# Performance work log

Hardware: AMD Instinct MI355X
Metric: run time of the kernel (lower is better)

## Reference

```python
import jax, jax.numpy as jnp
import numpy as np

B, L, R, F = 16, 64, 256, 64
LIG_NIN, REC_NIN, EIN, EEMB = 32, 40, 16, 16
DEG = 8
E_LIG, E_REC = B * L * DEG, B * R * DEG
NL = 3
PNAMES = ["emb_nW", "emb_nb", "emb_eW", "emb_eb", "hidW", "hidb", "ln0_g", "ln0_b",
          "efW", "efb", "convb", "outW", "outb", "lng", "lnb"]
INT_NAMES = ("lig_src", "lig_dst", "rec_src", "rec_dst")


def _lrelu(v):
    return jax.nn.leaky_relu(v, 0.01)


def _ln(x, g, b):
    m = x.mean(-1, keepdims=True)
    v = ((x - m) ** 2).mean(-1, keepdims=True)
    return (x - m) / jnp.sqrt(v + 1e-5) * g + b


def _side(node_x, edge_x, src, dst, n_nodes, p):
    # GraphEmbedding: linear node/edge embedding
    eh = edge_x @ p["emb_eW"] + p["emb_eb"]                      # [E, EEMB]
    h = _lrelu(node_x @ p["emb_nW"] + p["emb_nb"]) @ p["hidW"] + p["hidb"]
    h = _ln(h, p["ln0_g"], p["ln0_b"])                           # [N, F]
    deg = jax.ops.segment_sum(jnp.ones(src.shape[0], jnp.float32), dst, num_segments=n_nodes)
    deg = jnp.maximum(deg, 1.0)[:, None]
    prev = []
    for i in range(NL):
        hh = _lrelu(h)
        # NNConv: per-edge F x F weight conditioned on edge features
        We = (eh @ p["efW"][i] + p["efb"][i]).reshape(-1, F, F)  # [E, F, F]
        msg = jnp.einsum('ei,eio->eo', hh[src], We)              # [E, F]
        agg = jax.ops.segment_sum(msg, dst, num_segments=n_nodes) / deg + p["convb"][i]
        h = _ln(_lrelu(agg) @ p["outW"][i] + p["outb"][i], p["lng"][i], p["lnb"][i])
        if i >= 2:  # residual to layer i-2
            h = h + prev[i - 2]
        prev.append(h)
    return h


def _forward(fl, lig_src, lig_dst, rec_src, rec_dst):
    lig_p = {n: fl["lig_" + n] for n in PNAMES}
    rec_p = {n: fl["rec_" + n] for n in PNAMES}
    lig_h = _side(fl["lig_x"], fl["lig_e"], lig_src, lig_dst, B * L, lig_p)
    rec_h = _side(fl["rec_x"], fl["rec_e"], rec_src, rec_dst, B * R, rec_p)
    # per-graph einsum('lf,rf->lr') scoring, batched since graphs are equal-sized
    op = jnp.einsum('blf,brf->blr', lig_h.reshape(B, L, F), rec_h.reshape(B, R, F))
    out = op.mean((1, 2))
    return out, op


def setup_inputs() -> dict:
    key = jax.random.key(0)
    it = iter(jax.random.split(key, 80))
    def nrm(shape, s=0.1):
        return jax.random.normal(next(it), shape, jnp.float32) * s
    inp = {}
    inp["lig_x"] = nrm((B * L, LIG_NIN), 1.0)
    inp["rec_x"] = nrm((B * R, REC_NIN), 1.0)
    inp["lig_e"] = nrm((E_LIG, EIN), 1.0)
    inp["rec_e"] = nrm((E_REC, EIN), 1.0)
    def edges(npg, epg, k1, k2):
        offs = (jnp.arange(B) * npg)[:, None]
        s = (jax.random.randint(k1, (B, epg), 0, npg) + offs).reshape(-1).astype(jnp.int32)
        d = (jax.random.randint(k2, (B, epg), 0, npg) + offs).reshape(-1).astype(jnp.int32)
        return s, d
    inp["lig_src"], inp["lig_dst"] = edges(L, L * DEG, next(it), next(it))
    inp["rec_src"], inp["rec_dst"] = edges(R, R * DEG, next(it), next(it))
    for pre, nin in (("lig", LIG_NIN), ("rec", REC_NIN)):
        inp[pre + "_emb_nW"] = nrm((nin, F)); inp[pre + "_emb_nb"] = nrm((F,))
        inp[pre + "_emb_eW"] = nrm((EIN, EEMB)); inp[pre + "_emb_eb"] = nrm((EEMB,))
        inp[pre + "_hidW"] = nrm((F, F)); inp[pre + "_hidb"] = nrm((F,))
        inp[pre + "_ln0_g"] = jnp.ones((F,)); inp[pre + "_ln0_b"] = jnp.zeros((F,))
        inp[pre + "_efW"] = nrm((NL, EEMB, F * F), 0.05); inp[pre + "_efb"] = nrm((NL, F * F), 0.05)
        inp[pre + "_convb"] = nrm((NL, F))
        inp[pre + "_outW"] = nrm((NL, F, F)); inp[pre + "_outb"] = nrm((NL, F))
        inp[pre + "_lng"] = jnp.ones((NL, F)); inp[pre + "_lnb"] = jnp.zeros((NL, F))
    return inp


def reference(lig_x, rec_x, lig_e, rec_e, lig_src, lig_dst, rec_src, rec_dst,
              lig_emb_nW, lig_emb_nb, lig_emb_eW, lig_emb_eb, lig_hidW, lig_hidb,
              lig_ln0_g, lig_ln0_b, lig_efW, lig_efb, lig_convb, lig_outW, lig_outb,
              lig_lng, lig_lnb,
              rec_emb_nW, rec_emb_nb, rec_emb_eW, rec_emb_eb, rec_hidW, rec_hidb,
              rec_ln0_g, rec_ln0_b, rec_efW, rec_efb, rec_convb, rec_outW, rec_outb,
              rec_lng, rec_lnb):
    all_args = dict(locals())
    fl = {k: v for k, v in all_args.items() if k not in INT_NAMES}
    return _forward(fl, lig_src, lig_dst, rec_src, rec_dst)
```

## Files before the change

kernel.cpp:

```cpp
#include <hip/hip_runtime.h>
#include <hip/hip_bf16.h>

#define NLIG 1024
#define NREC 4096
#define NTOT 5120
#define ELIG 8192
#define ETOT 40960
#define TPAD 1092

typedef __bf16 bf16x8 __attribute__((ext_vector_type(8)));
typedef float f32x4 __attribute__((ext_vector_type(4)));

struct Params {
  const float *lig_x, *rec_x, *lig_e, *rec_e;
  const int *lig_src, *lig_dst, *rec_src, *rec_dst;
  const float *nW[2], *nb[2], *eW[2], *eb[2], *hW[2], *hb[2], *g0[2], *b0[2];
  const float *efW[2], *efb[2], *convb[2], *outW[2], *outb[2], *lng[2], *lnb[2];
  float *aggA, *aggB, *prev0;
  __bf16 *eh, *Abf, *Wp, *oWp;
  int *deg;
  unsigned *bkt;
  int *bktbase, *bktcnt;
  float *out;
};

__device__ __forceinline__ float lrelu(float v){ return v > 0.f ? v : 0.01f * v; }

__device__ __forceinline__ float wsum(float v){
  #pragma unroll
  for (int off = 32; off > 0; off >>= 1) v += __shfl_xor(v, off, 64);
  return v;
}

__device__ __forceinline__ void window(int bid, int& side, int& r0, int& gr0,
                                       int& ebase, int& ecnt, int& egbase,
                                       const int*& srcArr, const int*& dstArr,
                                       const Params& p){
  if (bid < 64){
    side = 0; int b = bid >> 2, w = bid & 3;
    r0 = b*64 + w*16; gr0 = r0; ebase = b*512; ecnt = 512; egbase = ebase;
    srcArr = p.lig_src; dstArr = p.lig_dst;
  } else {
    side = 1; int g = bid - 64; int b = g >> 4, w = g & 15;
    r0 = b*256 + w*16; gr0 = NLIG + r0; ebase = b*2048; ecnt = 2048; egbase = ELIG + ebase;
    srcArr = p.rec_src; dstArr = p.rec_dst;
  }
}

__global__ __launch_bounds__(1024) void k_pre(Params p){
  __shared__ float sW[2][256], sb[2][16];
  __shared__ float nwl[40*64];
  __shared__ float hwl[64*64];
  __shared__ float sx[16][40], st[16][64];
  __shared__ int scnt[16], sbase[16], scur[16], dcnt[16];
  const int tid = threadIdx.x, bid = blockIdx.x;
  const int lane = tid & 63, wid = tid >> 6;
  const int gtid = bid*1024 + tid;

  int side, r0, gr0, ebase, ecnt, egbase;
  const int *srcArr, *dstArr;
  window(bid, side, r0, gr0, ebase, ecnt, egbase, srcArr, dstArr, p);
  const int nin = side ? 40 : 32;

  if (tid < 256){ sW[0][tid] = p.eW[0][tid]; sW[1][tid] = p.eW[1][tid]; }
  if (tid < 16){ sb[0][tid] = p.eb[0][tid]; sb[1][tid] = p.eb[1][tid];
                 scnt[tid] = 0; dcnt[tid] = 0; }
  for (int i = tid; i < nin*64; i += 1024) nwl[i] = p.nW[side][i];
  for (int i = tid; i < 4096; i += 1024) hwl[i] = p.hW[side][i];
  __syncthreads();

  if (gtid < 52224){
    int l  = gtid & 63;
    int t2 = gtid >> 6;
    int kk = t2 & 1;
    int t3 = t2 >> 1;
    int ct = t3 % 68;
    int sl = t3 / 68;
    int sd = sl / 3, ly = sl % 3;
    int ocol = ct*16 + (l & 15);
    int kslot = ocol >> 6, oo = ocol & 63;
    const float* src = (kslot < 16)
        ? (p.efW[sd] + (size_t)ly*16*4096 + (size_t)kslot*4096)
        : (p.efb[sd] + (size_t)ly*4096);
    bf16x8 w;
    #pragma unroll
    for (int j = 0; j < 8; j++){
      int i = kk*32 + (l >> 4)*8 + j;
      w[j] = (__bf16)src[i*64 + oo];
    }
    ((bf16x8*)p.Wp)[(size_t)sl*68*2*64 + (ct*2 + kk)*64 + l] = w;
  } else if (gtid < 52224 + 3072){
    int id2 = gtid - 52224;
    int l = id2 & 63;
    int t2 = id2 >> 6;
    int kk = t2 & 1;
    int ct = (t2 >> 1) & 3;
    int sl = t2 >> 3;
    int sd = sl / 3, ly = sl % 3;
    const float* src = p.outW[sd] + (size_t)ly*4096;
    bf16x8 w;
    #pragma unroll
    for (int j = 0; j < 8; j++){
      int i = kk*32 + (l >> 4)*8 + j;
      w[j] = (__bf16)src[i*64 + ct*16 + (l & 15)];
    }
    ((bf16x8*)p.oWp)[(size_t)(sl*8 + ct*2 + kk)*64 + l] = w;
  }

  if (gtid < ETOT){
    int e = gtid;
    int esd = e >= ELIG;
    int el = esd ? e - ELIG : e;
    const float* ex = (esd ? p.rec_e : p.lig_e) + (size_t)el * 16;
    float x[16];
    #pragma unroll
    for (int j = 0; j < 16; j += 4){
      float4 v = *(const float4*)(ex + j);
      x[j] = v.x; x[j+1] = v.y; x[j+2] = v.z; x[j+3] = v.w;
    }
    bf16x8 s0, s1;
    #pragma unroll
    for (int k = 0; k < 16; k++){
      float acc = sb[esd][k];
      #pragma unroll
      for (int j = 0; j < 16; j++) acc += x[j] * sW[esd][j*16 + k];
      if (k < 8) s0[k] = (__bf16)acc; else s1[k-8] = (__bf16)acc;
    }
    bf16x8* ehp = (bf16x8*)(p.eh + (size_t)e * 16);
    ehp[0] = s0; ehp[1] = s1;
  }

  for (int i = gtid; i < NTOT*64; i += 320*1024){ p.aggA[i] = 0.f; p.aggB[i] = 0.f; }
  if (gtid < 16) p.out[gtid] = 0.f;

  {
    int n = gr0 + wid;
    int nl = r0 + wid;
    const float* x = (side ? p.rec_x : p.lig_x) + (size_t)nl * nin;
    if (lane < nin) sx[wid][lane] = x[lane];
    float tv = p.nb[side][lane];
    for (int j = 0; j < nin; j++) tv += sx[wid][j] * nwl[j*64 + lane];
    st[wid][lane] = lrelu(tv);
    float hv = p.hb[side][lane];
    #pragma unroll 8
    for (int j = 0; j < 64; j++) hv += st[wid][j] * hwl[j*64 + lane];
    float m = wsum(hv) * (1.f/64.f);
    float d = hv - m;
    float v = wsum(d*d) * (1.f/64.f);
    float o = d * rsqrtf(v + 1e-5f) * p.g0[side][lane] + p.b0[side][lane];
    p.Abf[(size_t)n*64 + lane] = (__bf16)lrelu(o);
  }

  for (int i = tid; i < ecnt; i += 1024){
    int s = srcArr[ebase + i];
    if ((unsigned)(s - r0) < 16u) atomicAdd(&scnt[s - r0], 1);
    int d = dstArr[ebase + i];
    if ((unsigned)(d - r0) < 16u) atomicAdd(&dcnt[d - r0], 1);
  }
  __syncthreads();
  if (tid < 64){
    int v = (lane < 16) ? scnt[lane] : 0;
    int pre = v;
    #pragma unroll
    for (int off = 1; off < 16; off <<= 1){
      int u = __shfl_up(pre, off, 64);
      if (lane >= off) pre += u;
    }
    if (lane < 16){ sbase[lane] = pre - v; scur[lane] = pre - v; }
  }
  if (tid < 16) p.deg[gr0 + tid] = dcnt[tid];
  __syncthreads();
  for (int i = tid; i < ecnt; i += 1024){
    int s = srcArr[ebase + i];
    if ((unsigned)(s - r0) < 16u){
      int d = dstArr[ebase + i];
      int pos = atomicAdd(&scur[s - r0], 1);
      p.bkt[(size_t)bid*2048 + pos] = ((unsigned)d << 16) | (unsigned)i;
    }
  }
  if (tid < 16){ p.bktbase[bid*16 + tid] = sbase[tid]; p.bktcnt[bid*16 + tid] = scnt[tid]; }
}

__global__ __launch_bounds__(1024, 8) void k_layer(Params p, int layer){
  const int tid = threadIdx.x, bid = blockIdx.x;
  const int lane = tid & 63, wid = tid >> 6;
  int side, r0, gr0, ebase, ecnt, egbase;
  const int *srcArr, *dstArr;
  window(bid, side, r0, gr0, ebase, ecnt, egbase, srcArr, dstArr, p);
  float* aggR = (layer == 1) ? p.aggA : p.aggB;
  float* aggW = (layer == 1) ? p.aggB : p.aggA;

  const int myDeg  = p.deg[gr0 + wid];
  const int myCnt  = p.bktcnt[bid*16 + wid];
  const int myBase = p.bktbase[bid*16 + wid];

  __shared__ __bf16 Tl[16][TPAD];
  __shared__ __bf16 albf[16][64];
  __shared__ __bf16 sabf[16][64];
  __shared__ float updo[16][68];

  if (layer > 0){
    int lm1 = layer - 1;
    int n = gr0 + wid;
    float a = aggR[(size_t)n*64 + lane];
    aggR[(size_t)n*64 + lane] = 0.f;
    float dg = fmaxf((float)myDeg, 1.f);
    a = lrelu(a / dg + p.convb[side][lm1*64 + lane]);
    sabf[wid][lane] = (__bf16)a;
    __syncthreads();
    if (wid < 4){
      int ct = wid;
      bf16x8 a0u, a1u;
      #pragma unroll
      for (int j = 0; j < 8; j++){
        a0u[j] = sabf[lane & 15][(lane >> 4)*8 + j];
        a1u[j] = sabf[lane & 15][32 + (lane >> 4)*8 + j];
      }
      const bf16x8* Ob = (const bf16x8*)p.oWp + (size_t)(side*3 + lm1)*8*64;
      bf16x8 b0 = Ob[(ct*2 + 0)*64 + lane];
      bf16x8 b1 = Ob[(ct*2 + 1)*64 + lane];
      f32x4 d = {0.f, 0.f, 0.f, 0.f};
      d = __builtin_amdgcn_mfma_f32_16x16x32_bf16(a0u, b0, d, 0, 0, 0);
      d = __builtin_amdgcn_mfma_f32_16x16x32_bf16(a1u, b1, d, 0, 0, 0);
      int orw = (lane >> 4)*4, ocl = ct*16 + (lane & 15);
      updo[orw+0][ocl] = d[0];
      updo[orw+1][ocl] = d[1];
      updo[orw+2][ocl] = d[2];
      updo[orw+3][ocl] = d[3];
    }
    __syncthreads();
    {
      float hv = p.outb[side][lm1*64 + lane] + updo[wid][lane];
      float m = wsum(hv) * (1.f/64.f);
      float d = hv - m;
      float v = wsum(d*d) * (1.f/64.f);
      float o = d * rsqrtf(v + 1e-5f) * p.lng[side][lm1*64 + lane] + p.lnb[side][lm1*64 + lane];
      if (layer == 1) p.prev0[(size_t)n*64 + lane] = o;
      albf[wid][lane] = (__bf16)lrelu(o);
    }
  }
  __syncthreads();

  bf16x8 a0, a1;
  if (layer == 0){
    const bf16x8* A = (const bf16x8*)(p.Abf + (size_t)(gr0 + (lane & 15))*64 + (lane >> 4)*8);
    a0 = A[0]; a1 = A[4];
  } else {
    #pragma unroll
    for (int j = 0; j < 8; j++){
      a0[j] = albf[lane & 15][(lane >> 4)*8 + j];
      a1[j] = albf[lane & 15][32 + (lane >> 4)*8 + j];
    }
  }
  const bf16x8* Wb = (const bf16x8*)p.Wp + (size_t)(side*3 + layer)*68*2*64;
  int orow = (lane >> 4)*4, ocol = lane & 15;
  {
    int ct = wid;
    bf16x8 b0 = Wb[(ct*2 + 0)*64 + lane];
    bf16x8 b1 = Wb[(ct*2 + 1)*64 + lane];
    while (ct < 68){
      int ctn = ct + 16;
      bf16x8 nb0 = b0, nb1 = b1;
      if (ctn < 68){ nb0 = Wb[(ctn*2 + 0)*64 + lane]; nb1 = Wb[(ctn*2 + 1)*64 + lane]; }
      f32x4 d = {0.f, 0.f, 0.f, 0.f};
      d = __builtin_amdgcn_mfma_f32_16x16x32_bf16(a0, b0, d, 0, 0, 0);
      d = __builtin_amdgcn_mfma_f32_16x16x32_bf16(a1, b1, d, 0, 0, 0);
      int col = ct*16 + ocol;
      Tl[orow+0][col] = (__bf16)d[0];
      Tl[orow+1][col] = (__bf16)d[1];
      Tl[orow+2][col] = (__bf16)d[2];
      Tl[orow+3][col] = (__bf16)d[3];
      b0 = nb0; b1 = nb1; ct = ctn;
    }
  }
  __syncthreads();

  if (myCnt > 0){
    float t[17];
    #pragma unroll
    for (int k = 0; k < 17; k++) t[k] = (float)Tl[wid][k*64 + lane];
    size_t base = (size_t)bid*2048 + myBase;
    for (int c0 = 0; c0 < myCnt; c0 += 64){
      int nn = min(64, myCnt - c0);
      unsigned ew = (lane < nn) ? p.bkt[base + c0 + lane] : 0u;
      auto doe = [&](unsigned v, bf16x8 e0, bf16x8 e1){
        int gd = (int)(v >> 16) + (side ? NLIG : 0);
        float m = t[16];
        #pragma unroll
        for (int k = 0; k < 8; k++) m += (float)e0[k] * t[k];
        #pragma unroll
        for (int k = 0; k < 8; k++) m += (float)e1[k] * t[8+k];
        atomicAdd(&aggW[(size_t)gd*64 + lane], m);
      };
      auto rowp = [&](unsigned v){
        return (const bf16x8*)(p.eh + (size_t)(egbase + (int)(v & 0xffffu))*16);
      };
      int j = 0;
      for (; j + 4 <= nn; j += 4){
        unsigned v0 = __shfl(ew, j, 64),   v1 = __shfl(ew, j+1, 64);
        unsigned v2 = __shfl(ew, j+2, 64), v3 = __shfl(ew, j+3, 64);
        const bf16x8 *p0 = rowp(v0), *p1 = rowp(v1), *p2 = rowp(v2), *p3 = rowp(v3);
        bf16x8 a0e = p0[0], a1e = p0[1], b0e = p1[0], b1e = p1[1];
        bf16x8 c0e = p2[0], c1e = p2[1], d0e = p3[0], d1e = p3[1];
        doe(v0, a0e, a1e); doe(v1, b0e, b1e); doe(v2, c0e, c1e); doe(v3, d0e, d1e);
      }
      for (; j < nn; j++){
        unsigned v0 = __shfl(ew, j, 64);
        const bf16x8* pp = rowp(v0);
        doe(v0, pp[0], pp[1]);
      }
    }
  }
}

__global__ __launch_bounds__(1024) void k_final(Params p){
  const int tid = threadIdx.x, bid = blockIdx.x;
  const int lane = tid & 63, wid = tid >> 6;
  int b = bid >> 4, rt = bid & 15;
  __shared__ float slh[64][65];
  __shared__ float srh[16][65];
  __shared__ float owl[2][4096];
  __shared__ float sa[16][64];
  __shared__ float ps[16];

  for (int idx = tid; idx < 4096; idx += 1024){
    owl[0][idx] = p.outW[0][2*4096 + idx];
    owl[1][idx] = p.outW[1][2*4096 + idx];
  }
  __syncthreads();

  for (int rr = wid; rr < 80; rr += 16){
    int side = rr >= 64;
    int n = side ? (NLIG + b*256 + rt*16 + (rr - 64)) : (b*64 + rr);
    float a = p.aggA[(size_t)n*64 + lane];
    float dg = fmaxf((float)p.deg[n], 1.f);
    a = lrelu(a / dg + p.convb[side][128 + lane]);
    sa[wid][lane] = a;
    float hv = p.outb[side][128 + lane];
    const float* ow = &owl[side][0];
    #pragma unroll 8
    for (int j = 0; j < 64; j++) hv += sa[wid][j] * ow[j*64 + lane];
    float m = wsum(hv) * (1.f/64.f);
    float d = hv - m;
    float v = wsum(d*d) * (1.f/64.f);
    float o = d * rsqrtf(v + 1e-5f) * p.lng[side][128 + lane] + p.lnb[side][128 + lane];
    o += p.prev0[(size_t)n*64 + lane];
    if (side) srh[rr - 64][lane] = o; else slh[rr][lane] = o;
  }
  __syncthreads();

  int r = tid & 15, lg = tid >> 4;
  float acc = 0.f;
  #pragma unroll 8
  for (int f = 0; f < 64; f++) acc += slh[lg][f] * srh[r][f];
  p.out[16 + (size_t)b*16384 + (size_t)lg*256 + rt*16 + r] = acc;

  float psum = wsum(acc);
  if (lane == 0) ps[wid] = psum;
  __syncthreads();
  if (tid == 0){
    float s = 0.f;
    #pragma unroll
    for (int i = 0; i < 16; i++) s += ps[i];
    atomicAdd(&p.out[b], s * (1.f/16384.f));
  }
}

extern "C" void kernel_launch(void* const* d_in, const int* in_sizes, int n_in,
                              void* d_out, int out_size, void* d_ws, size_t ws_size,
                              hipStream_t stream){
  Params p;
  p.lig_x  = (const float*)d_in[0];
  p.rec_x  = (const float*)d_in[1];
  p.lig_e  = (const float*)d_in[2];
  p.rec_e  = (const float*)d_in[3];
  p.lig_src = (const int*)d_in[4];
  p.lig_dst = (const int*)d_in[5];
  p.rec_src = (const int*)d_in[6];
  p.rec_dst = (const int*)d_in[7];
  for (int s = 0; s < 2; s++){
    const int o = 8 + s*15;
    p.nW[s]   = (const float*)d_in[o+0];  p.nb[s]   = (const float*)d_in[o+1];
    p.eW[s]   = (const float*)d_in[o+2];  p.eb[s]   = (const float*)d_in[o+3];
    p.hW[s]   = (const float*)d_in[o+4];  p.hb[s]   = (const float*)d_in[o+5];
    p.g0[s]   = (const float*)d_in[o+6];  p.b0[s]   = (const float*)d_in[o+7];
    p.efW[s]  = (const float*)d_in[o+8];  p.efb[s]  = (const float*)d_in[o+9];
    p.convb[s]= (const float*)d_in[o+10]; p.outW[s] = (const float*)d_in[o+11];
    p.outb[s] = (const float*)d_in[o+12]; p.lng[s]  = (const float*)d_in[o+13];
    p.lnb[s]  = (const float*)d_in[o+14];
  }
  char* W = (char*)d_ws;
  p.aggA  = (float*)W;  W += (size_t)NTOT*64*4;
  p.aggB  = (float*)W;  W += (size_t)NTOT*64*4;
  p.prev0 = (float*)W;  W += (size_t)NTOT*64*4;
  p.eh    = (__bf16*)W; W += (size_t)ETOT*16*2;
  p.Abf   = (__bf16*)W; W += (size_t)NTOT*64*2;
  p.Wp    = (__bf16*)W; W += (size_t)2*3*68*2*64*8*2;
  p.oWp   = (__bf16*)W; W += (size_t)2*3*4*2*64*8*2;
  p.deg   = (int*)W;    W += (size_t)NTOT*4;
  p.bkt   = (unsigned*)W; W += (size_t)320*2048*4;
  p.bktbase = (int*)W;  W += (size_t)320*16*4;
  p.bktcnt  = (int*)W;  W += (size_t)320*16*4;
  p.out   = (float*)d_out;

  k_pre<<<320, 1024, 0, stream>>>(p);
  k_layer<<<320, 1024, 0, stream>>>(p, 0);
  k_layer<<<320, 1024, 0, stream>>>(p, 1);
  k_layer<<<320, 1024, 0, stream>>>(p, 2);
  k_final<<<256, 1024, 0, stream>>>(p);
}
```

Baseline: 95.35 us.

## Fuse preprocessing with layer-0 message passing into a single front kernel

Merges the pre-pass kernel and the layer-0 kernel into one k_front kernel. It computes node embeddings in shared memory instead of staging them through global Abf, and builds the per-edge embeddings only for edges in each block's bucket. Layer 0's weight tile is built directly from fp32 efW with an MFMA, and its messages are scattered using the shared edge list. Agg zeroing moves to hipMemsetAsync and the first weight tile load is hoisted in k_mid. This removes one kernel launch and a global round trip, at the cost of repeated per-block conversion of efW and more serialized work per block.

```diff
diff --git a/kernel.cpp b/kernel.cpp
--- a/kernel.cpp
+++ b/kernel.cpp
@@ -17,7 +17,7 @@
   const float *nW[2], *nb[2], *eW[2], *eb[2], *hW[2], *hb[2], *g0[2], *b0[2];
   const float *efW[2], *efb[2], *convb[2], *outW[2], *outb[2], *lng[2], *lnb[2];
   float *aggA, *aggB, *prev0;
-  __bf16 *eh, *Abf, *Wp, *oWp;
+  __bf16 *eh, *Wp, *oWp;
   int *deg;
   unsigned *bkt;
   int *bktbase, *bktcnt;
@@ -47,12 +47,18 @@
   }
 }
 
-__global__ __launch_bounds__(1024) void k_pre(Params p){
-  __shared__ float sW[2][256], sb[2][16];
-  __shared__ float nwl[40*64];
-  __shared__ float hwl[64*64];
-  __shared__ float sx[16][40], st[16][64];
+__global__ __launch_bounds__(1024, 8) void k_front(Params p){
+  union EmbT {
+    struct { float nwl[40*64], hwl[64*64], sx[16][40], st[16][64]; } e;
+    __bf16 Tl[16][TPAD];
+  };
+  __shared__ EmbT su;
+  __shared__ float sW[256], sb[16];
+  __shared__ __bf16 albf[16][64];
+  __shared__ unsigned elist[2048];
   __shared__ int scnt[16], sbase[16], scur[16], dcnt[16];
+  __shared__ int sTot;
+
   const int tid = threadIdx.x, bid = blockIdx.x;
   const int lane = tid & 63, wid = tid >> 6;
   const int gtid = bid*1024 + tid;
@@ -62,11 +68,11 @@
   window(bid, side, r0, gr0, ebase, ecnt, egbase, srcArr, dstArr, p);
   const int nin = side ? 40 : 32;
 
-  if (tid < 256){ sW[0][tid] = p.eW[0][tid]; sW[1][tid] = p.eW[1][tid]; }
-  if (tid < 16){ sb[0][tid] = p.eb[0][tid]; sb[1][tid] = p.eb[1][tid];
-                 scnt[tid] = 0; dcnt[tid] = 0; }
-  for (int i = tid; i < nin*64; i += 1024) nwl[i] = p.nW[side][i];
-  for (int i = tid; i < 4096; i += 1024) hwl[i] = p.hW[side][i];
+  if (tid < 256) sW[tid] = p.eW[side][tid];
+  if (tid < 16){ sb[tid] = p.eb[side][tid]; scnt[tid] = 0; dcnt[tid] = 0; }
+  for (int i = tid; i < nin*64; i += 1024) su.e.nwl[i] = p.nW[side][i];
+  for (int i = tid; i < 4096; i += 1024) su.e.hwl[i] = p.hW[side][i];
+  if (gtid < 16) p.out[gtid] = 0.f;
   __syncthreads();
 
   if (gtid < 52224){
@@ -107,50 +113,6 @@
     ((bf16x8*)p.oWp)[(size_t)(sl*8 + ct*2 + kk)*64 + l] = w;
   }
 
-  if (gtid < ETOT){
-    int e = gtid;
-    int esd = e >= ELIG;
-    int el = esd ? e - ELIG : e;
-    const float* ex = (esd ? p.rec_e : p.lig_e) + (size_t)el * 16;
-    float x[16];
-    #pragma unroll
-    for (int j = 0; j < 16; j += 4){
-      float4 v = *(const float4*)(ex + j);
-      x[j] = v.x; x[j+1] = v.y; x[j+2] = v.z; x[j+3] = v.w;
-    }
-    bf16x8 s0, s1;
-    #pragma unroll
-    for (int k = 0; k < 16; k++){
-      float acc = sb[esd][k];
-      #pragma unroll
-      for (int j = 0; j < 16; j++) acc += x[j] * sW[esd][j*16 + k];
-      if (k < 8) s0[k] = (__bf16)acc; else s1[k-8] = (__bf16)acc;
-    }
-    bf16x8* ehp = (bf16x8*)(p.eh + (size_t)e * 16);
-    ehp[0] = s0; ehp[1] = s1;
-  }
-
-  for (int i = gtid; i < NTOT*64; i += 320*1024){ p.aggA[i] = 0.f; p.aggB[i] = 0.f; }
-  if (gtid < 16) p.out[gtid] = 0.f;
-
-  {
-    int n = gr0 + wid;
-    int nl = r0 + wid;
-    const float* x = (side ? p.rec_x : p.lig_x) + (size_t)nl * nin;
-    if (lane < nin) sx[wid][lane] = x[lane];
-    float tv = p.nb[side][lane];
-    for (int j = 0; j < nin; j++) tv += sx[wid][j] * nwl[j*64 + lane];
-    st[wid][lane] = lrelu(tv);
-    float hv = p.hb[side][lane];
-    #pragma unroll 8
-    for (int j = 0; j < 64; j++) hv += st[wid][j] * hwl[j*64 + lane];
-    float m = wsum(hv) * (1.f/64.f);
-    float d = hv - m;
-    float v = wsum(d*d) * (1.f/64.f);
-    float o = d * rsqrtf(v + 1e-5f) * p.g0[side][lane] + p.b0[side][lane];
-    p.Abf[(size_t)n*64 + lane] = (__bf16)lrelu(o);
-  }
-
   for (int i = tid; i < ecnt; i += 1024){
     int s = srcArr[ebase + i];
     if ((unsigned)(s - r0) < 16u) atomicAdd(&scnt[s - r0], 1);
@@ -167,6 +129,7 @@
       if (lane >= off) pre += u;
     }
     if (lane < 16){ sbase[lane] = pre - v; scur[lane] = pre - v; }
+    if (lane == 15) sTot = pre;
   }
   if (tid < 16) p.deg[gr0 + tid] = dcnt[tid];
   __syncthreads();
@@ -175,13 +138,129 @@
     if ((unsigned)(s - r0) < 16u){
       int d = dstArr[ebase + i];
       int pos = atomicAdd(&scur[s - r0], 1);
-      p.bkt[(size_t)bid*2048 + pos] = ((unsigned)d << 16) | (unsigned)i;
+      unsigned v = ((unsigned)d << 16) | (unsigned)i;
+      elist[pos] = v;
+      p.bkt[(size_t)bid*2048 + pos] = v;
     }
   }
   if (tid < 16){ p.bktbase[bid*16 + tid] = sbase[tid]; p.bktcnt[bid*16 + tid] = scnt[tid]; }
-}
-
-__global__ __launch_bounds__(1024, 8) void k_layer(Params p, int layer){
+
+  {
+    int nl = r0 + wid;
+    const float* x = (side ? p.rec_x : p.lig_x) + (size_t)nl * nin;
+    if (lane < nin) su.e.sx[wid][lane] = x[lane];
+    float tv = p.nb[side][lane];
+    for (int j = 0; j < nin; j++) tv += su.e.sx[wid][j] * su.e.nwl[j*64 + lane];
+    su.e.st[wid][lane] = lrelu(tv);
+    float hv = p.hb[side][lane];
+    #pragma unroll 8
+    for (int j = 0; j < 64; j++) hv += su.e.st[wid][j] * su.e.hwl[j*64 + lane];
+    float m = wsum(hv) * (1.f/64.f);
+    float d = hv - m;
+    float v = wsum(d*d) * (1.f/64.f);
+    float o = d * rsqrtf(v + 1e-5f) * p.g0[side][lane] + p.b0[side][lane];
+    albf[wid][lane] = (__bf16)lrelu(o);
+  }
+  __syncthreads();
+
+  {
+    int total = sTot;
+    const float* exb = side ? p.rec_e : p.lig_e;
+    for (int t2 = tid; t2 < total; t2 += 1024){
+      int el = (int)(elist[t2] & 0xffffu);
+      const float* ex = exb + (size_t)(ebase + el) * 16;
+      float x[16];
+      #pragma unroll
+      for (int j = 0; j < 16; j += 4){
+        float4 v = *(const float4*)(ex + j);
+        x[j] = v.x; x[j+1] = v.y; x[j+2] = v.z; x[j+3] = v.w;
+      }
+      bf16x8 s0, s1;
+      #pragma unroll
+      for (int k = 0; k < 16; k++){
+        float acc = sb[k];
+        #pragma unroll
+        for (int j = 0; j < 16; j++) acc += x[j] * sW[j*16 + k];
+        if (k < 8) s0[k] = (__bf16)acc; else s1[k-8] = (__bf16)acc;
+      }
+      bf16x8* ehp = (bf16x8*)(p.eh + (size_t)(egbase + el) * 16);
+      ehp[0] = s0; ehp[1] = s1;
+    }
+  }
+  __threadfence_block();
+  __syncthreads();
+
+  {
+    bf16x8 a0, a1;
+    #pragma unroll
+    for (int j = 0; j < 8; j++){
+      a0[j] = albf[lane & 15][(lane >> 4)*8 + j];
+      a1[j] = albf[lane & 15][32 + (lane >> 4)*8 + j];
+    }
+    const float* W0 = p.efW[side];
+    const float* B0 = p.efb[side];
+    int orow = (lane >> 4)*4, ocol = lane & 15;
+    for (int ct = wid; ct < 68; ct += 16){
+      int oc = ct*16 + ocol;
+      int kslot = oc >> 6, oo = oc & 63;
+      const float* src = (kslot < 16) ? (W0 + (size_t)kslot*4096) : B0;
+      bf16x8 b0, b1;
+      #pragma unroll
+      for (int j = 0; j < 8; j++){
+        int i0 = (lane >> 4)*8 + j;
+        b0[j] = (__bf16)src[(size_t)i0*64 + oo];
+        b1[j] = (__bf16)src[(size_t)(32 + i0)*64 + oo];
+      }
+      f32x4 d = {0.f, 0.f, 0.f, 0.f};
+      d = __builtin_amdgcn_mfma_f32_16x16x32_bf16(a0, b0, d, 0, 0, 0);
+      d = __builtin_amdgcn_mfma_f32_16x16x32_bf16(a1, b1, d, 0, 0, 0);
+      int col = ct*16 + ocol;
+      su.Tl[orow+0][col] = (__bf16)d[0];
+      su.Tl[orow+1][col] = (__bf16)d[1];
+      su.Tl[orow+2][col] = (__bf16)d[2];
+      su.Tl[orow+3][col] = (__bf16)d[3];
+    }
+  }
+  __syncthreads();
+
+  {
+    int cnt = scnt[wid];
+    if (cnt > 0){
+      float t[17];
+      #pragma unroll
+      for (int k = 0; k < 17; k++) t[k] = (float)su.Tl[wid][k*64 + lane];
+      int base = sbase[wid];
+      auto doe = [&](unsigned v, bf16x8 e0, bf16x8 e1){
+        int gd = (int)(v >> 16) + (side ? NLIG : 0);
+        float m = t[16];
+        #pragma unroll
+        for (int k = 0; k < 8; k++) m += (float)e0[k] * t[k];
+        #pragma unroll
+        for (int k = 0; k < 8; k++) m += (float)e1[k] * t[8+k];
+        atomicAdd(&p.aggA[(size_t)gd*64 + lane], m);
+      };
+      auto rowp = [&](unsigned v){
+        return (const bf16x8*)(p.eh + (size_t)(egbase + (int)(v & 0xffffu))*16);
+      };
+      int j = 0;
+      for (; j + 4 <= cnt; j += 4){
+        unsigned v0 = elist[base+j],   v1 = elist[base+j+1];
+        unsigned v2 = elist[base+j+2], v3 = elist[base+j+3];
+        const bf16x8 *p0 = rowp(v0), *p1 = rowp(v1), *p2 = rowp(v2), *p3 = rowp(v3);
+        bf16x8 a0e = p0[0], a1e = p0[1], b0e = p1[0], b1e = p1[1];
+        bf16x8 c0e = p2[0], c1e = p2[1], d0e = p3[0], d1e = p3[1];
+        doe(v0, a0e, a1e); doe(v1, b0e, b1e); doe(v2, c0e, c1e); doe(v3, d0e, d1e);
+      }
+      for (; j < cnt; j++){
+        unsigned v0 = elist[base+j];
+        const bf16x8* pp = rowp(v0);
+        doe(v0, pp[0], pp[1]);
+      }
+    }
+  }
+}
+
+__global__ __launch_bounds__(1024, 8) void k_mid(Params p, int layer){
   const int tid = threadIdx.x, bid = blockIdx.x;
   const int lane = tid & 63, wid = tid >> 6;
   int side, r0, gr0, ebase, ecnt, egbase;
@@ -193,13 +272,16 @@
   const int myDeg  = p.deg[gr0 + wid];
   const int myCnt  = p.bktcnt[bid*16 + wid];
   const int myBase = p.bktbase[bid*16 + wid];
+  const bf16x8* Wb = (const bf16x8*)p.Wp + (size_t)(side*3 + layer)*68*2*64;
+  bf16x8 pb0 = Wb[(wid*2 + 0)*64 + lane];
+  bf16x8 pb1 = Wb[(wid*2 + 1)*64 + lane];
 
   __shared__ __bf16 Tl[16][TPAD];
   __shared__ __bf16 albf[16][64];
   __shared__ __bf16 sabf[16][64];
   __shared__ float updo[16][68];
 
-  if (layer > 0){
+  {
     int lm1 = layer - 1;
     int n = gr0 + wid;
     float a = aggR[(size_t)n*64 + lane];
@@ -241,23 +323,16 @@
   }
   __syncthreads();
 
-  bf16x8 a0, a1;
-  if (layer == 0){
-    const bf16x8* A = (const bf16x8*)(p.Abf + (size_t)(gr0 + (lane & 15))*64 + (lane >> 4)*8);
-    a0 = A[0]; a1 = A[4];
-  } else {
+  {
+    bf16x8 a0, a1;
     #pragma unroll
     for (int j = 0; j < 8; j++){
       a0[j] = albf[lane & 15][(lane >> 4)*8 + j];
       a1[j] = albf[lane & 15][32 + (lane >> 4)*8 + j];
     }
-  }
-  const bf16x8* Wb = (const bf16x8*)p.Wp + (size_t)(side*3 + layer)*68*2*64;
-  int orow = (lane >> 4)*4, ocol = lane & 15;
-  {
+    int orow = (lane >> 4)*4, ocol = lane & 15;
     int ct = wid;
-    bf16x8 b0 = Wb[(ct*2 + 0)*64 + lane];
-    bf16x8 b1 = Wb[(ct*2 + 1)*64 + lane];
+    bf16x8 b0 = pb0, b1 = pb1;
     while (ct < 68){
       int ctn = ct + 16;
       bf16x8 nb0 = b0, nb1 = b1;
@@ -394,7 +469,6 @@
   p.aggB  = (float*)W;  W += (size_t)NTOT*64*4;
   p.prev0 = (float*)W;  W += (size_t)NTOT*64*4;
   p.eh    = (__bf16*)W; W += (size_t)ETOT*16*2;
-  p.Abf   = (__bf16*)W; W += (size_t)NTOT*64*2;
   p.Wp    = (__bf16*)W; W += (size_t)2*3*68*2*64*8*2;
   p.oWp   = (__bf16*)W; W += (size_t)2*3*4*2*64*8*2;
   p.deg   = (int*)W;    W += (size_t)NTOT*4;
@@ -403,9 +477,10 @@
   p.bktcnt  = (int*)W;  W += (size_t)320*16*4;
   p.out   = (float*)d_out;
 
-  k_pre<<<320, 1024, 0, stream>>>(p);
-  k_layer<<<320, 1024, 0, stream>>>(p, 0);
-  k_layer<<<320, 1024, 0, stream>>>(p, 1);
-  k_layer<<<320, 1024, 0, stream>>>(p, 2);
+  hipMemsetAsync(p.aggA, 0, (size_t)2*NTOT*64*sizeof(float), stream);
+
+  k_front<<<320, 1024, 0, stream>>>(p);
+  k_mid<<<320, 1024, 0, stream>>>(p, 1);
+  k_mid<<<320, 1024, 0, stream>>>(p, 2);
   k_final<<<256, 1024, 0, stream>>>(p);
 }
```

Measured after the change: 120.2 us. 1.26x slower.
